# Performance work log

Measured on AMD Instinct MI355X. Metric: run time of the kernel, lower is better.

## Reference

```python
import jax, jax.numpy as jnp
import numpy as np

B, V, T = 64, 196, 64       # batch, visual tokens, text tokens
VIS, TXT, E = 768, 768, 512  # backbone dims, joint embed dim


def l2norm(x):
    return x / jnp.maximum(jnp.linalg.norm(x, axis=-1, keepdims=True), 1e-12)


def setup_inputs() -> dict:
    key = jax.random.key(0)
    ks = jax.random.split(key, 16)
    f = lambda k, s: jax.random.normal(k, s, dtype=jnp.float32)
    return {
        'v_cls': f(ks[0], (B, VIS)),
        'v_tok': f(ks[1], (B, V, VIS)),
        't_cls': f(ks[2], (B, TXT)),
        't_tok': f(ks[3], (B, T, TXT)),
        'Wv_cls': f(ks[4], (VIS, E)) * 0.02, 'bv_cls': jnp.zeros((E,), jnp.float32),
        'Wt_cls': f(ks[5], (TXT, E)) * 0.02, 'bt_cls': jnp.zeros((E,), jnp.float32),
        'Wv_tok': f(ks[6], (VIS, E)) * 0.02, 'bv_tok': jnp.zeros((E,), jnp.float32),
        'Wt_tok': f(ks[7], (TXT, E)) * 0.02, 'bt_tok': jnp.zeros((E,), jnp.float32),
        'wv_fc': f(ks[8], (E,)) * 0.02, 'bv_fc': jnp.zeros((), jnp.float32),
        'wt_fc': f(ks[9], (E,)) * 0.02, 'bt_fc': jnp.zeros((), jnp.float32),
        'text_length': jax.random.randint(ks[10], (B,), 16, T + 1),
    }


def reference(v_cls, v_tok, t_cls, t_tok,
              Wv_cls, bv_cls, Wt_cls, bt_cls,
              Wv_tok, bv_tok, Wt_tok, bt_tok,
              wv_fc, bv_fc, wt_fc, bt_fc, text_length):
    ve_cls = v_cls @ Wv_cls + bv_cls
    te_cls = t_cls @ Wt_cls + bt_cls
    ve = v_tok @ Wv_tok + bv_tok          # [B, V, E]
    te = t_tok @ Wt_tok + bt_tok          # [B, T, E]

    # per-token scalar weights (Linear(E, 1).squeeze(2))
    vw = ve @ wv_fc + bv_fc               # [B, V]
    tw = te @ wt_fc + bt_fc               # [B, T]

    # mask padded text positions (pos >= length), then softmax
    pad = jnp.arange(T)[None, :] >= text_length[:, None]
    tw = jax.nn.softmax(jnp.where(pad, -jnp.inf, tw), axis=-1)
    vw = jax.nn.softmax(vw, axis=-1)

    ve = l2norm(ve)
    te = l2norm(te)

    # full cross-batch token similarity [b, q, v, t]
    sim = jnp.einsum('bvd,qtd->bqvt', ve, te)
    image_to_text = jnp.einsum('bqv,bv->bq', sim.max(axis=-1), vw)
    text_to_image = jnp.einsum('bqt,qt->bq', sim.max(axis=2), tw)

    # diagonal (b == q) similarities drive the cdcr gathers
    sim_diag = jnp.einsum('bvd,btd->bvt', ve, te)
    idx1 = jnp.argmax(sim_diag, axis=-1)   # [B, V] best text token per visual token
    idx2 = jnp.argmax(sim_diag, axis=1)    # [B, T] best visual token per text token
    max_v = jnp.take_along_axis(ve, idx2[:, :, None], axis=1).reshape(-1, E)  # [B*T, E]
    max_t = jnp.take_along_axis(te, idx1[:, :, None], axis=1).reshape(-1, E)  # [B*V, E]

    t_feat = te.reshape(-1, E)
    v_feat = ve.reshape(-1, E)

    def zn(x):  # torch .std() is unbiased (ddof=1)
        return (x - x.mean(axis=0)) / jnp.std(x, axis=0, ddof=1)

    c1 = jnp.einsum('ac,ad,a->cd', zn(t_feat), zn(max_v), tw.reshape(-1)) / B
    c2 = jnp.einsum('ac,ad,a->cd', zn(v_feat), zn(max_t), vw.reshape(-1)) / B
    c = (c1 + c2) / 2.0

    D = c.shape[0]
    on_diag = jnp.sum((jnp.diagonal(c) - 1.0) ** 2)
    off_diag = jnp.sum(c.reshape(-1)[1:].reshape(D - 1, D + 1)[:, :-1] ** 2)
    cdcr_loss = 0.1 * (on_diag * 1.0 + off_diag * 0.06)

    return image_to_text, text_to_image, cdcr_loss
```

## Files before the change

### kernel.cpp

```cpp
#include <hip/hip_runtime.h>
#include <cstddef>

#define EDIM 512
#define KDIM 768
#define NB 64
#define NV 196
#define NT 64
#define MROWS_V (NB * NV)
#define MROWS_T (NB * NT)

typedef __attribute__((ext_vector_type(8))) short bf16x8;
typedef __attribute__((ext_vector_type(4))) float f32x4;

static __device__ inline unsigned short f2bf(float f) {
  unsigned u = __float_as_uint(f);
  unsigned r = (u + 0x7fff + ((u >> 16) & 1)) >> 16;
  return (unsigned short)r;
}
static __device__ inline float bf2f(short s) {
  return __uint_as_float(((unsigned)(unsigned short)s) << 16);
}
static __device__ __forceinline__ int swz4(int r) { return (r + (r >> 2)) & 3; }

static __device__ __forceinline__ void gload16(const void* g, void* l) {
  __builtin_amdgcn_global_load_lds(
      (const __attribute__((address_space(1))) void*)g,
      (__attribute__((address_space(3))) void*)l, 16, 0, 0);
}

__global__ void k_prep(const float* __restrict__ va, short* __restrict__ vo, int na8,
                       const float* __restrict__ ta, short* __restrict__ to, int nb8,
                       const float* __restrict__ W0, const float* __restrict__ W1,
                       short* __restrict__ T0, short* __restrict__ T1) {
  __shared__ float tile[32][33];
  int blk = blockIdx.x;
  int tid = threadIdx.x;
  if (blk < 6240) {
    int i = blk * 256 + tid;
    const float* in; short* outp; int idx;
    if (i < na8) { in = va; outp = vo; idx = i; }
    else { idx = i - na8; if (idx >= nb8) return; in = ta; outp = to; }
    float4 a = *(const float4*)(in + (size_t)idx * 8);
    float4 b = *(const float4*)(in + (size_t)idx * 8 + 4);
    bf16x8 v;
    v[0] = (short)f2bf(a.x); v[1] = (short)f2bf(a.y);
    v[2] = (short)f2bf(a.z); v[3] = (short)f2bf(a.w);
    v[4] = (short)f2bf(b.x); v[5] = (short)f2bf(b.y);
    v[6] = (short)f2bf(b.z); v[7] = (short)f2bf(b.w);
    *(bf16x8*)(outp + (size_t)idx * 8) = v;
  } else {
    int z = blk - 6240;
    int bx = z % 24, by = (z / 24) % 16, bz = z / 384;
    const float* W = bz ? W1 : W0;
    short*       T = bz ? T1 : T0;
    int k0 = bx * 32, n0 = by * 32;
    int tx = tid & 31, ty = tid >> 5;
    for (int i = ty; i < 32; i += 8)
      tile[i][tx] = W[(size_t)(k0 + i) * EDIM + n0 + tx];
    __syncthreads();
    for (int i = ty; i < 32; i += 8)
      T[(size_t)(n0 + i) * KDIM + k0 + tx] = (short)f2bf(tile[tx][i]);
  }
}

__global__ __launch_bounds__(256, 4) void k_proj_mfma2(
    const short* __restrict__ vX, const short* __restrict__ tX,
    const short* __restrict__ WvT, const short* __restrict__ WtT,
    const float* __restrict__ vb, const float* __restrict__ tb,
    short* __restrict__ vout, short* __restrict__ tout) {
  __shared__ short As[2][128 * 32];
  __shared__ short Bs[2][128 * 32];
  int y = blockIdx.y;
  const short* Xbf; const short* WT; const float* bias; short* Mbf; int r0;
  if (y < 98) { Xbf = vX; WT = WvT; bias = vb; Mbf = vout; r0 = y * 128; }
  else        { Xbf = tX; WT = WtT; bias = tb; Mbf = tout; r0 = (y - 98) * 128; }
  int n0 = blockIdx.x * 128;
  int tid = threadIdx.x;
  int w = tid >> 6, lane = tid & 63, lg = lane >> 4, li = lane & 15;
  int fsw = (li + (li >> 2)) & 3;

  const short* aSrc[2];
  const short* bSrc[2];
#pragma unroll
  for (int uu = 0; uu < 2; ++uu) {
    int u = uu * 256 + w * 64 + lane;
    int row = u >> 2, seg = u & 3;
    int ss = seg ^ swz4(row);
    aSrc[uu] = Xbf + (size_t)(r0 + row) * KDIM + ss * 8;
    bSrc[uu] = WT + (size_t)(n0 + row) * KDIM + ss * 8;
  }

  auto stage = [&](int bb) {
    short* Ad = &As[bb][0];
    short* Bd = &Bs[bb][0];
#pragma unroll
    for (int uu = 0; uu < 2; ++uu) {
      gload16(aSrc[uu], Ad + (uu * 256 + w * 64) * 8);
      aSrc[uu] += 32;
      gload16(bSrc[uu], Bd + (uu * 256 + w * 64) * 8);
      bSrc[uu] += 32;
    }
  };

  f32x4 acc[2][8];
#pragma unroll
  for (int i = 0; i < 2; ++i)
#pragma unroll
    for (int j = 0; j < 8; ++j) acc[i][j] = (f32x4){0.f, 0.f, 0.f, 0.f};

  stage(0);
  int cur = 0;
  const int NKC = KDIM / 32;
  for (int kc = 0; kc < NKC; ++kc) {
    __builtin_amdgcn_s_barrier();
    if (kc < NKC - 1) {
      stage(cur ^ 1);
      asm volatile("s_waitcnt vmcnt(4)" ::: "memory");
    } else {
      asm volatile("s_waitcnt vmcnt(0)" ::: "memory");
    }
    __builtin_amdgcn_s_barrier();
    const short* Ab = &As[cur][0];
    const short* Bb = &Bs[cur][0];
    bf16x8 bfr[8];
#pragma unroll
    for (int j = 0; j < 8; ++j)
      bfr[j] = *(const bf16x8*)(Bb + (j * 16 + li) * 32 + (lg ^ fsw) * 8);
    __builtin_amdgcn_s_setprio(1);
#pragma unroll
    for (int i = 0; i < 2; ++i) {
      bf16x8 afr = *(const bf16x8*)(Ab + ((w * 2 + i) * 16 + li) * 32 + (lg ^ fsw) * 8);
#pragma unroll
      for (int j = 0; j < 8; ++j)
        acc[i][j] = __builtin_amdgcn_mfma_f32_16x16x32_bf16(afr, bfr[j], acc[i][j], 0, 0, 0);
    }
    __builtin_amdgcn_s_setprio(0);
    cur ^= 1;
  }
#pragma unroll
  for (int j = 0; j < 8; ++j) {
    int n = n0 + j * 16 + li;
    float bb = bias[n];
#pragma unroll
    for (int i = 0; i < 2; ++i)
#pragma unroll
      for (int reg = 0; reg < 4; ++reg)
        Mbf[(size_t)(r0 + (w * 2 + i) * 16 + lg * 4 + reg) * EDIM + n] =
            (short)f2bf(acc[i][j][reg] + bb);
  }
}

__global__ void k_normfc2(short* __restrict__ vM, short* __restrict__ tM,
                          const float* __restrict__ vfcw, const float* __restrict__ tfcw,
                          const float* __restrict__ vfcb, const float* __restrict__ tfcb,
                          float* __restrict__ vwout, float* __restrict__ twout) {
  int blk = blockIdx.x;
  short* Mbf; const float* fcw; const float* fcb; float* wout; int row;
  if (blk < 3136) { Mbf = vM; fcw = vfcw; fcb = vfcb; wout = vwout;
                    row = blk * 4 + (threadIdx.x >> 6); if (row >= 12544) return; }
  else            { Mbf = tM; fcw = tfcw; fcb = tfcb; wout = twout;
                    row = (blk - 3136) * 4 + (threadIdx.x >> 6); if (row >= 4096) return; }
  int lane = threadIdx.x & 63;
  short* p = Mbf + (size_t)row * EDIM + lane * 8;
  bf16x8 v = *(bf16x8*)p;
  float4 w0 = *(const float4*)(fcw + lane * 8);
  float4 w1 = *(const float4*)(fcw + lane * 8 + 4);
  float a[8];
#pragma unroll
  for (int j = 0; j < 8; ++j) a[j] = bf2f(v[j]);
  float dot = a[0] * w0.x + a[1] * w0.y + a[2] * w0.z + a[3] * w0.w +
              a[4] * w1.x + a[5] * w1.y + a[6] * w1.z + a[7] * w1.w;
  float ss = a[0] * a[0] + a[1] * a[1] + a[2] * a[2] + a[3] * a[3] +
             a[4] * a[4] + a[5] * a[5] + a[6] * a[6] + a[7] * a[7];
  for (int s = 1; s < 64; s <<= 1) {
    dot += __shfl_xor(dot, s);
    ss += __shfl_xor(ss, s);
  }
  float inv = 1.0f / fmaxf(sqrtf(ss), 1e-12f);
#pragma unroll
  for (int j = 0; j < 8; ++j) v[j] = (short)f2bf(a[j] * inv);
  *(bf16x8*)p = v;
  if (lane == 0) wout[row] = dot + fcb[0];
}

__global__ void k_softmax(float* __restrict__ vwf, float* __restrict__ twf,
                          const int* __restrict__ tlen) {
  __shared__ float red[8];
  int tid = threadIdx.x;
  if (blockIdx.x < 64) {
    int b = blockIdx.x;
    float x = (tid < NV) ? vwf[b * NV + tid] : -1e30f;
    float m = x;
    for (int s = 1; s < 64; s <<= 1) m = fmaxf(m, __shfl_xor(m, s));
    if ((tid & 63) == 0) red[tid >> 6] = m;
    __syncthreads();
    m = fmaxf(fmaxf(red[0], red[1]), fmaxf(red[2], red[3]));
    float e = (tid < NV) ? expf(x - m) : 0.0f;
    float s = e;
    for (int st = 1; st < 64; st <<= 1) s += __shfl_xor(s, st);
    if ((tid & 63) == 0) red[4 + (tid >> 6)] = s;
    __syncthreads();
    s = red[4] + red[5] + red[6] + red[7];
    if (tid < NV) vwf[b * NV + tid] = e / s;
  } else {
    int b = blockIdx.x - 64;
    if (tid < 64) {
      int len = tlen[b];
      float x = twf[b * NT + tid];
      bool valid = tid < len;
      float xv = valid ? x : -1e30f;
      float m = xv;
      for (int s = 1; s < 64; s <<= 1) m = fmaxf(m, __shfl_xor(m, s));
      float e = valid ? expf(x - m) : 0.0f;
      float s = e;
      for (int st = 1; st < 64; st <<= 1) s += __shfl_xor(s, st);
      twf[b * NT + tid] = e / s;
    }
  }
}

__global__ __launch_bounds__(512, 4) void k_sim(
    const short* __restrict__ ve_bf, const short* __restrict__ te_bf,
    const float* __restrict__ vwf, const float* __restrict__ twf,
    float* __restrict__ out, int* __restrict__ gMT, int* __restrict__ gMV) {
  __shared__ short As[2][208 * 32];
  __shared__ short Bs[2][128 * 32];
  __shared__ float colv[8][64];
  __shared__ int   coli[8][64];
  __shared__ float redp[8];
  int n = blockIdx.x;
  int xcd = n & 7, idx = n >> 3;
  int b = xcd * 8 + (idx & 7);
  int qq = idx >> 3;
  int tid = threadIdx.x;
  int w = tid >> 6, lane = tid & 63, lg = lane >> 4, li = lane & 15;
  int qsel = w >> 2, wr = w & 3;
  int q = 2 * qq + qsel;
  const short* Abf = ve_bf + (size_t)b * NV * EDIM;
  const short* Bbf = te_bf + (size_t)qq * 128 * EDIM;
  int fsw = (li + (li >> 2)) & 3;
  int nt = wr ? 3 : 4;
  int tbase = wr ? (1 + wr * 3) : 0;

  const short* aSrc[2];
#pragma unroll
  for (int uu = 0; uu < 2; ++uu) {
    int u = uu * 512 + w * 64 + lane;
    int row = u >> 2;
    if (row > NV - 1) row = NV - 1;
    int seg = u & 3;
    int ss = seg ^ swz4(row);
    aSrc[uu] = Abf + (size_t)row * EDIM + ss * 8;
  }
  const short* bSrc;
  {
    int u = tid;
    int row = u >> 2, seg = u & 3;
    int ss = seg ^ swz4(row);
    bSrc = Bbf + (size_t)row * EDIM + ss * 8;
  }

  auto stage = [&](int bb) {
    short* Ad = &As[bb][0];
    short* Bd = &Bs[bb][0];
    gload16(bSrc, Bd + (w * 64) * 8);
    bSrc += 32;
#pragma unroll
    for (int uu = 0; uu < 2; ++uu) {
      int u0 = uu * 512 + w * 64;
      if (u0 < NV * 4) {
        gload16(aSrc[uu], Ad + u0 * 8);
        aSrc[uu] += 32;
      }
    }
  };

  f32x4 acc[4][4];
#pragma unroll
  for (int i = 0; i < 4; ++i)
#pragma unroll
    for (int j = 0; j < 4; ++j) acc[i][j] = (f32x4){0.f, 0.f, 0.f, 0.f};

  stage(0);
  int cur = 0;
  for (int kc = 0; kc < 16; ++kc) {
    __builtin_amdgcn_s_barrier();
    if (kc < 15) {
      stage(cur ^ 1);
      if (w <= 4) asm volatile("s_waitcnt vmcnt(3)" ::: "memory");
      else        asm volatile("s_waitcnt vmcnt(2)" ::: "memory");
    } else {
      asm volatile("s_waitcnt vmcnt(0)" ::: "memory");
    }
    __builtin_amdgcn_s_barrier();
    const short* Ab2 = &As[cur][0];
    const short* Bb2 = &Bs[cur][0];
    bf16x8 bfr[4];
#pragma unroll
    for (int j = 0; j < 4; ++j)
      bfr[j] = *(const bf16x8*)(Bb2 + (qsel * 64 + j * 16 + li) * 32 + (lg ^ fsw) * 8);
    __builtin_amdgcn_s_setprio(1);
#pragma unroll
    for (int i = 0; i < 4; ++i) {
      if (i < nt) {
        bf16x8 afr = *(const bf16x8*)(Ab2 + ((tbase + i) * 16 + li) * 32 + (lg ^ fsw) * 8);
#pragma unroll
        for (int j = 0; j < 4; ++j)
          acc[i][j] = __builtin_amdgcn_mfma_f32_16x16x32_bf16(afr, bfr[j], acc[i][j], 0, 0, 0);
      }
    }
    __builtin_amdgcn_s_setprio(0);
    cur ^= 1;
  }

  bool diag = (b == q);
  bool diagblk = (b >> 1) == qq;
  float ip = 0.f;

  if (diagblk) {
#pragma unroll
    for (int i = 0; i < 4; ++i) {
      if (i < nt) {
#pragma unroll
        for (int reg = 0; reg < 4; ++reg) {
          int v = (tbase + i) * 16 + lg * 4 + reg;
          float m = acc[i][0][reg];
          int ti = li;
#pragma unroll
          for (int j = 1; j < 4; ++j) {
            float vv = acc[i][j][reg];
            int t = j * 16 + li;
            if (vv > m) { m = vv; ti = t; }
          }
          for (int d = 1; d < 16; d <<= 1) {
            float om = __shfl_xor(m, d);
            int oi = __shfl_xor(ti, d);
            if (om > m || (om == m && oi < ti)) { m = om; ti = oi; }
          }
          if (li == 0 && v < NV) {
            ip += vwf[b * NV + v] * m;
            if (diag) gMT[b * NV + v] = b * NT + ti;
          }
        }
      }
    }
    float cm[4]; int cv[4];
#pragma unroll
    for (int j = 0; j < 4; ++j) { cm[j] = -3.0e38f; cv[j] = 0; }
#pragma unroll
    for (int i = 0; i < 4; ++i) {
      if (i < nt) {
#pragma unroll
        for (int reg = 0; reg < 4; ++reg) {
          int v = (tbase + i) * 16 + lg * 4 + reg;
          bool ok = v < NV;
#pragma unroll
          for (int j = 0; j < 4; ++j) {
            float s = ok ? acc[i][j][reg] : -3.0e38f;
            if (s > cm[j]) { cm[j] = s; cv[j] = v; }
          }
        }
      }
    }
#pragma unroll
    for (int j = 0; j < 4; ++j) {
      for (int d = 16; d < 64; d <<= 1) {
        float om = __shfl_xor(cm[j], d);
        int ov = __shfl_xor(cv[j], d);
        if (om > cm[j] || (om == cm[j] && ov < cv[j])) { cm[j] = om; cv[j] = ov; }
      }
      if (lg == 0) { colv[w][j * 16 + li] = cm[j]; coli[w][j * 16 + li] = cv[j]; }
    }
  } else {
#pragma unroll
    for (int i = 0; i < 4; ++i) {
      if (i < nt) {
#pragma unroll
        for (int reg = 0; reg < 4; ++reg) {
          int v = (tbase + i) * 16 + lg * 4 + reg;
          float m = fmaxf(fmaxf(acc[i][0][reg], acc[i][1][reg]),
                          fmaxf(acc[i][2][reg], acc[i][3][reg]));
          for (int d = 1; d < 16; d <<= 1) m = fmaxf(m, __shfl_xor(m, d));
          if (li == 0 && v < NV) ip += vwf[b * NV + v] * m;
        }
      }
    }
    float cm[4];
#pragma unroll
    for (int j = 0; j < 4; ++j) cm[j] = -3.0e38f;
#pragma unroll
    for (int i = 0; i < 4; ++i) {
      if (i < nt) {
#pragma unroll
      for (int reg = 0; reg < 4; ++reg) {
          int v = (tbase + i) * 16 + lg * 4 + reg;
          bool ok = v < NV;
#pragma unroll
          for (int j = 0; j < 4; ++j)
            cm[j] = fmaxf(cm[j], ok ? acc[i][j][reg] : -3.0e38f);
        }
      }
    }
#pragma unroll
    for (int j = 0; j < 4; ++j) {
      for (int d = 16; d < 64; d <<= 1) cm[j] = fmaxf(cm[j], __shfl_xor(cm[j], d));
      if (lg == 0) colv[w][j * 16 + li] = cm[j];
    }
  }
  for (int d = 1; d < 64; d <<= 1) ip += __shfl_xor(ip, d);
  if (lane == 0) redp[w] = ip;
  __syncthreads();
  if (tid < 128) {
    int qs = tid >> 6, t = tid & 63;
    int qe = 2 * qq + qs;
    float m = colv[qs * 4][t];
    if (diagblk) {
      int bi = coli[qs * 4][t];
#pragma unroll
      for (int w2 = 1; w2 < 4; ++w2) {
        float om = colv[qs * 4 + w2][t];
        int ov = coli[qs * 4 + w2][t];
        if (om > m || (om == m && ov < bi)) { m = om; bi = ov; }
      }
      if (b == qe) gMV[b * NT + t] = b * NV + bi;
    } else {
#pragma unroll
      for (int w2 = 1; w2 < 4; ++w2) m = fmaxf(m, colv[qs * 4 + w2][t]);
    }
    float p = twf[qe * NT + t] * m;
    for (int d = 1; d < 64; d <<= 1) p += __shfl_xor(p, d);
    if ((tid & 63) == 0) out[4096 + b * 64 + qe] = p;
  }
  if (tid == 0) {
    out[b * 64 + 2 * qq]     = redp[0] + redp[1] + redp[2] + redp[3];
    out[b * 64 + 2 * qq + 1] = redp[4] + redp[5] + redp[6] + redp[7];
  }
}

__global__ void k_materialize(const short* __restrict__ ve_bf, const short* __restrict__ te_bf,
                              const int* __restrict__ gMT, const int* __restrict__ gMV,
                              const float* __restrict__ vwf, const float* __restrict__ twf,
                              short* __restrict__ tTw, short* __restrict__ mvT,
                              short* __restrict__ vTw, short* __restrict__ mtT,
                              float* __restrict__ statPart) {
  int z = blockIdx.z;
  int at = blockIdx.x, ct = blockIdx.y;
  int K = (z == 2 || z == 3) ? MROWS_V : MROWS_T;
  if (at * 64 >= K) return;
  const short* src; const int* g = 0; short* dst;
  bool applyW;
  const float* wS = (z <= 1) ? twf : vwf;
  if (z == 0)      { src = te_bf; dst = tTw; applyW = true;  }
  else if (z == 1) { src = ve_bf; g = gMV; dst = mvT; applyW = false; }
  else if (z == 2) { src = ve_bf; dst = vTw; applyW = true;  }
  else             { src = te_bf; g = gMT; dst = mtT; applyW = false; }
  __shared__ float tile[64][67];
  __shared__ float wrow[64];
  int tid = threadIdx.x;
  for (int u = tid; u < 512; u += 256) {
    int a = u >> 3, cseg = (u & 7) << 3;
    int ga = at * 64 + a;
    int row = g ? g[ga] : ga;
    bf16x8 vv = *(const bf16x8*)(src + (size_t)row * EDIM + ct * 64 + cseg);
#pragma unroll
    for (int j = 0; j < 8; j++) tile[a][cseg + j] = bf2f(vv[j]);
    if ((u & 7) == 0) wrow[a] = wS[ga];
  }
  __syncthreads();
  for (int u = tid; u < 512; u += 256) {
    int c = u >> 3, aseg = (u & 7) << 3;
    bf16x8 ov;
#pragma unroll
    for (int j = 0; j < 8; j++) {
      float x = tile[aseg + j][c];
      if (applyW) x *= wrow[aseg + j];
      ov[j] = (short)f2bf(x);
    }
    *(bf16x8*)(dst + (size_t)(ct * 64 + c) * K + at * 64 + aseg) = ov;
  }
  int cl = tid >> 2, part = tid & 3;
  float s = 0, ssq = 0, sw = 0;
  for (int a = part * 16; a < part * 16 + 16; ++a) {
    float x = tile[a][cl];
    s += x; ssq += x * x; sw += wrow[a] * x;
  }
  for (int d = 1; d < 4; d <<= 1) {
    s += __shfl_xor(s, d); ssq += __shfl_xor(ssq, d); sw += __shfl_xor(sw, d);
  }
  if (part == 0) {
    int cbase = (z == 0) ? 0 : (z == 1) ? 64 : (z == 2) ? 128 : 324;
    size_t sidx = ((size_t)(cbase + at) * 512 + ct * 64 + cl) * 3;
    statPart[sidx] = s; statPart[sidx + 1] = ssq; statPart[sidx + 2] = sw;
  }
}

__global__ void k_statfin(const float* __restrict__ statPart, float* __restrict__ stats) {
  int m = blockIdx.x, c = threadIdx.x;
  int R = (m < 2) ? MROWS_T : MROWS_V;
  int nchunk = (m < 2) ? 64 : 196;
  int base = (m == 0) ? 0 : (m == 1) ? 64 : (m == 2) ? 128 : 324;
  float s = 0, ss = 0, sw = 0;
  for (int ch = 0; ch < nchunk; ch++) {
    size_t idx = ((size_t)(base + ch) * 512 + c) * 3;
    s += statPart[idx]; ss += statPart[idx + 1]; sw += statPart[idx + 2];
  }
  float mean = s / R;
  float var = (ss - s * mean) / (R - 1);
  float rstd = 1.0f / sqrtf(var);
  stats[(m * 3 + 0) * 512 + c] = mean;
  stats[(m * 3 + 1) * 512 + c] = rstd;
  stats[(m * 3 + 2) * 512 + c] = sw;
}

__global__ __launch_bounds__(256, 4) void k_wgemm2(
    const short* __restrict__ tTw, const short* __restrict__ mvT,
    const short* __restrict__ vTw, const short* __restrict__ mtT,
    float* __restrict__ Spart) {
  __shared__ short As[2][128 * 32];
  __shared__ short Bs[2][128 * 32];
  int c0 = blockIdx.x * 128, d0 = blockIdx.y * 128;
  int z = blockIdx.z;
  int which = z >> 3, slice = z & 7;
  const short* A = which ? vTw : tTw;
  const short* B = which ? mtT : mvT;
  int K = which ? MROWS_V : MROWS_T;
  int nch = (K >> 3) >> 5;
  int a0 = slice * (K >> 3);
  int tid = threadIdx.x;
  int w = tid >> 6, lane = tid & 63, lg = lane >> 4, li = lane & 15;
  int fsw = (li + (li >> 2)) & 3;

  const short* aSrc[2];
  const short* bSrc[2];
#pragma unroll
  for (int uu = 0; uu < 2; ++uu) {
    int u = uu * 256 + w * 64 + lane;
    int row = u >> 2, seg = u & 3;
    int ss = seg ^ swz4(row);
    aSrc[uu] = A + (size_t)(c0 + row) * K + a0 + ss * 8;
    bSrc[uu] = B + (size_t)(d0 + row) * K + a0 + ss * 8;
  }

  auto stage = [&](int bb) {
    short* Ad = &As[bb][0];
    short* Bd = &Bs[bb][0];
#pragma unroll
    for (int uu = 0; uu < 2; ++uu) {
      gload16(aSrc[uu], Ad + (uu * 256 + w * 64) * 8);
      aSrc[uu] += 32;
      gload16(bSrc[uu], Bd + (uu * 256 + w * 64) * 8);
      bSrc[uu] += 32;
    }
  };

  f32x4 acc[2][8];
#pragma unroll
  for (int i = 0; i < 2; ++i)
#pragma unroll
    for (int j = 0; j < 8; ++j) acc[i][j] = (f32x4){0.f, 0.f, 0.f, 0.f};

  stage(0);
  int cur = 0;
  for (int ch = 0; ch < nch; ++ch) {
    __builtin_amdgcn_s_barrier();
    if (ch < nch - 1) {
      stage(cur ^ 1);
      asm volatile("s_waitcnt vmcnt(4)" ::: "memory");
    } else {
      asm volatile("s_waitcnt vmcnt(0)" ::: "memory");
    }
    __builtin_amdgcn_s_barrier();
    const short* Ab = &As[cur][0];
    const short* Bb = &Bs[cur][0];
    bf16x8 bfr[8];
#pragma unroll
    for (int j = 0; j < 8; ++j)
      bfr[j] = *(const bf16x8*)(Bb + (j * 16 + li) * 32 + (lg ^ fsw) * 8);
    __builtin_amdgcn_s_setprio(1);
#pragma unroll
    for (int i = 0; i < 2; ++i) {
      bf16x8 afr = *(const bf16x8*)(Ab + ((w * 2 + i) * 16 + li) * 32 + (lg ^ fsw) * 8);
#pragma unroll
      for (int j = 0; j < 8; ++j)
        acc[i][j] = __builtin_amdgcn_mfma_f32_16x16x32_bf16(afr, bfr[j], acc[i][j], 0, 0, 0);
    }
    __builtin_amdgcn_s_setprio(0);
    cur ^= 1;
  }
  float* outp = Spart + (size_t)z * 512 * 512;
#pragma unroll
  for (int j = 0; j < 8; ++j) {
    int d = d0 + j * 16 + li;
#pragma unroll
    for (int i = 0; i < 2; ++i)
#pragma unroll
      for (int reg = 0; reg < 4; ++reg)
        outp[(size_t)(c0 + (w * 2 + i) * 16 + lg * 4 + reg) * 512 + d] = acc[i][j][reg];
  }
}

__global__ void k_assemble(const float* __restrict__ Spart, const float* __restrict__ stats,
                           float* __restrict__ lossPart) {
  int c = blockIdx.x, tid = threadIdx.x;
  float muT = stats[0 * 512 + c], rsT = stats[1 * 512 + c], swT = stats[2 * 512 + c];
  float muV = stats[6 * 512 + c], rsV = stats[7 * 512 + c], swV = stats[8 * 512 + c];
  const float W = 64.0f, invB = 1.0f / 64.0f;
  float on = 0, off = 0;
  for (int d = tid; d < 512; d += 256) {
    float s1 = 0, s2 = 0;
    for (int sl = 0; sl < 8; sl++) {
      s1 += Spart[((size_t)sl * 512 + c) * 512 + d];
      s2 += Spart[((size_t)(8 + sl) * 512 + c) * 512 + d];
    }
    float muMV = stats[3 * 512 + d], rsMV = stats[4 * 512 + d], swMV = stats[5 * 512 + d];
    float muMT = stats[9 * 512 + d], rsMT = stats[10 * 512 + d], swMT = stats[11 * 512 + d];
    float c1 = (s1 - muT * swMV - muMV * swT + muT * muMV * W) * rsT * rsMV * invB;
    float c2 = (s2 - muV * swMT - muMT * swV + muV * muMT * W) * rsV * rsMT * invB;
    float cc = 0.5f * (c1 + c2);
    if (d == c) { float dd = cc - 1.0f; on += dd * dd; }
    else off += cc * cc;
  }
  __shared__ float r1[4], r2[4];
  for (int s = 1; s < 64; s <<= 1) { on += __shfl_xor(on, s); off += __shfl_xor(off, s); }
  if ((tid & 63) == 0) { r1[tid >> 6] = on; r2[tid >> 6] = off; }
  __syncthreads();
  if (tid == 0) {
    lossPart[c * 2] = r1[0] + r1[1] + r1[2] + r1[3];
    lossPart[c * 2 + 1] = r2[0] + r2[1] + r2[2] + r2[3];
  }
}

__global__ void k_loss(const float* __restrict__ lossPart, float* __restrict__ out) {
  int tid = threadIdx.x;
  float on = 0, off = 0;
  for (int i = tid; i < 512; i += 256) { on += lossPart[2 * i]; off += lossPart[2 * i + 1]; }
  __shared__ float r1[4], r2[4];
  for (int s = 1; s < 64; s <<= 1) { on += __shfl_xor(on, s); off += __shfl_xor(off, s); }
  if ((tid & 63) == 0) { r1[tid >> 6] = on; r2[tid >> 6] = off; }
  __syncthreads();
  if (tid == 0)
    out[8192] = 0.1f * ((r1[0] + r1[1] + r1[2] + r1[3]) +
                        0.06f * (r2[0] + r2[1] + r2[2] + r2[3]));
}

extern "C" void kernel_launch(void* const* d_in, const int* in_sizes, int n_in,
                              void* d_out, int out_size, void* d_ws, size_t ws_size,
                              hipStream_t stream) {
  (void)in_sizes; (void)n_in; (void)out_size; (void)ws_size;
  const float* v_tok  = (const float*)d_in[1];
  const float* t_tok  = (const float*)d_in[3];
  const float* Wv_tok = (const float*)d_in[8];
  const float* Wt_tok = (const float*)d_in[10];
  const float* bv_tok = (const float*)d_in[9];
  const float* bt_tok = (const float*)d_in[11];
  const float* wv_fc  = (const float*)d_in[12];
  const float* bv_fc  = (const float*)d_in[13];
  const float* wt_fc  = (const float*)d_in[14];
  const float* bt_fc  = (const float*)d_in[15];
  const int*   tlen   = (const int*)d_in[16];
  float* out = (float*)d_out;

  char* wsb = (char*)d_ws;
  short* v_tok_bf = (short*)wsb;
  short* t_tok_bf = v_tok_bf + (size_t)9633792;
  short* WvT      = t_tok_bf + (size_t)3145728;
  short* WtT      = WvT + (size_t)393216;
  short* tTw = (short*)wsb;
  short* mvT = tTw + (size_t)2097152;
  short* vTw = mvT + (size_t)2097152;
  short* ve_bf = (short*)(wsb + 27131904);
  short* te_bf = ve_bf + (size_t)6422528;
  float* Spart = (float*)(wsb + 27131904);
  short* mtT = (short*)(wsb + 44171264);
  float* vwf = (float*)(wsb + 57016320);
  float* twf = vwf + 12544;
  int* gMT = (int*)(twf + 4096);
  int* gMV = gMT + 12544;
  float* statPart = (float*)(gMV + 4096);
  float* stats = statPart + (size_t)520 * 512 * 3;
  float* lossPart = stats + 6144;

  k_prep<<<7008, 256, 0, stream>>>(v_tok, v_tok_bf, 1204224, t_tok, t_tok_bf, 393216,
                                   Wv_tok, Wt_tok, WvT, WtT);
  k_proj_mfma2<<<dim3(4, 130), 256, 0, stream>>>(v_tok_bf, t_tok_bf, WvT, WtT,
                                                 bv_tok, bt_tok, ve_bf, te_bf);
  k_normfc2<<<4160, 256, 0, stream>>>(ve_bf, te_bf, wv_fc, wt_fc, bv_fc, bt_fc, vwf, twf);
  k_softmax<<<128, 256, 0, stream>>>(vwf, twf, tlen);
  k_sim<<<2048, 512, 0, stream>>>(ve_bf, te_bf, vwf, twf, out, gMT, gMV);
  k_materialize<<<dim3(196, 8, 4), 256, 0, stream>>>(ve_bf, te_bf, gMT, gMV, vwf, twf,
                                                     tTw, mvT, vTw, mtT, statPart);
  k_statfin<<<4, 512, 0, stream>>>(statPart, stats);
  k_wgemm2<<<dim3(4, 4, 16), 256, 0, stream>>>(tTw, mvT, vTw, mtT, Spart);
  k_assemble<<<512, 256, 0, stream>>>(Spart, stats, lossPart);
  k_loss<<<1, 256, 0, stream>>>(lossPart, out);
}
```

Before: 246.7 us.

## Store transposed operands in K-chunked layout and widen wgemm blocks to 512 threads

New measurement: 247.0 us, median of 2. No clear change (+0.1%).

```diff
diff --git a/kernel.cpp b/kernel.cpp
--- a/kernel.cpp
+++ b/kernel.cpp
@@ -476,7 +476,8 @@
       if (applyW) x *= wrow[aseg + j];
       ov[j] = (short)f2bf(x);
     }
-    *(bf16x8*)(dst + (size_t)(ct * 64 + c) * K + at * 64 + aseg) = ov;
+    int kchunk = at * 2 + (aseg >> 5);
+    *(bf16x8*)(dst + ((size_t)kchunk * 512 + ct * 64 + c) * 32 + (aseg & 31)) = ov;
   }
   int cl = tid >> 2, part = tid & 3;
   float s = 0, ssq = 0, sw = 0;
@@ -512,7 +513,7 @@
   stats[(m * 3 + 2) * 512 + c] = sw;
 }
 
-__global__ __launch_bounds__(256, 4) void k_wgemm2(
+__global__ __launch_bounds__(512, 2) void k_wgemm2(
     const short* __restrict__ tTw, const short* __restrict__ mvT,
     const short* __restrict__ vTw, const short* __restrict__ mtT,
     float* __restrict__ Spart) {
@@ -525,39 +526,29 @@
   const short* B = which ? mtT : mvT;
   int K = which ? MROWS_V : MROWS_T;
   int nch = (K >> 3) >> 5;
-  int a0 = slice * (K >> 3);
+  size_t a0c = (size_t)slice * nch;
   int tid = threadIdx.x;
   int w = tid >> 6, lane = tid & 63, lg = lane >> 4, li = lane & 15;
   int fsw = (li + (li >> 2)) & 3;
 
-  const short* aSrc[2];
-  const short* bSrc[2];
-#pragma unroll
-  for (int uu = 0; uu < 2; ++uu) {
-    int u = uu * 256 + w * 64 + lane;
-    int row = u >> 2, seg = u & 3;
+  const short* aSrc; const short* bSrc;
+  {
+    int row = tid >> 2, seg = tid & 3;
     int ss = seg ^ swz4(row);
-    aSrc[uu] = A + (size_t)(c0 + row) * K + a0 + ss * 8;
-    bSrc[uu] = B + (size_t)(d0 + row) * K + a0 + ss * 8;
+    aSrc = A + (a0c * 512 + (size_t)(c0 + row)) * 32 + ss * 8;
+    bSrc = B + (a0c * 512 + (size_t)(d0 + row)) * 32 + ss * 8;
   }
 
   auto stage = [&](int bb) {
-    short* Ad = &As[bb][0];
-    short* Bd = &Bs[bb][0];
-#pragma unroll
-    for (int uu = 0; uu < 2; ++uu) {
-      gload16(aSrc[uu], Ad + (uu * 256 + w * 64) * 8);
-      aSrc[uu] += 32;
-      gload16(bSrc[uu], Bd + (uu * 256 + w * 64) * 8);
-      bSrc[uu] += 32;
-    }
+    gload16(aSrc, &As[bb][0] + (w * 64) * 8);
+    aSrc += 512 * 32;
+    gload16(bSrc, &Bs[bb][0] + (w * 64) * 8);
+    bSrc += 512 * 32;
   };
 
-  f32x4 acc[2][8];
-#pragma unroll
-  for (int i = 0; i < 2; ++i)
-#pragma unroll
-    for (int j = 0; j < 8; ++j) acc[i][j] = (f32x4){0.f, 0.f, 0.f, 0.f};
+  f32x4 acc[8];
+#pragma unroll
+  for (int j = 0; j < 8; ++j) acc[j] = (f32x4){0.f, 0.f, 0.f, 0.f};
 
   stage(0);
   int cur = 0;
@@ -565,24 +556,19 @@
     __builtin_amdgcn_s_barrier();
     if (ch < nch - 1) {
       stage(cur ^ 1);
-      asm volatile("s_waitcnt vmcnt(4)" ::: "memory");
+      asm volatile("s_waitcnt vmcnt(2)" ::: "memory");
     } else {
       asm volatile("s_waitcnt vmcnt(0)" ::: "memory");
     }
     __builtin_amdgcn_s_barrier();
     const short* Ab = &As[cur][0];
     const short* Bb = &Bs[cur][0];
-    bf16x8 bfr[8];
-#pragma unroll
-    for (int j = 0; j < 8; ++j)
-      bfr[j] = *(const bf16x8*)(Bb + (j * 16 + li) * 32 + (lg ^ fsw) * 8);
+    bf16x8 afr = *(const bf16x8*)(Ab + (w * 16 + li) * 32 + (lg ^ fsw) * 8);
     __builtin_amdgcn_s_setprio(1);
 #pragma unroll
-    for (int i = 0; i < 2; ++i) {
-      bf16x8 afr = *(const bf16x8*)(Ab + ((w * 2 + i) * 16 + li) * 32 + (lg ^ fsw) * 8);
-#pragma unroll
-      for (int j = 0; j < 8; ++j)
-        acc[i][j] = __builtin_amdgcn_mfma_f32_16x16x32_bf16(afr, bfr[j], acc[i][j], 0, 0, 0);
+    for (int j = 0; j < 8; ++j) {
+      bf16x8 bfr = *(const bf16x8*)(Bb + (j * 16 + li) * 32 + (lg ^ fsw) * 8);
+      acc[j] = __builtin_amdgcn_mfma_f32_16x16x32_bf16(afr, bfr, acc[j], 0, 0, 0);
     }
     __builtin_amdgcn_s_setprio(0);
     cur ^= 1;
@@ -592,10 +578,8 @@
   for (int j = 0; j < 8; ++j) {
     int d = d0 + j * 16 + li;
 #pragma unroll
-    for (int i = 0; i < 2; ++i)
-#pragma unroll
-      for (int reg = 0; reg < 4; ++reg)
-        outp[(size_t)(c0 + (w * 2 + i) * 16 + lg * 4 + reg) * 512 + d] = acc[i][j][reg];
+    for (int reg = 0; reg < 4; ++reg)
+      outp[(size_t)(c0 + w * 16 + lg * 4 + reg) * 512 + d] = acc[j][reg];
   }
 }
 
@@ -690,7 +674,7 @@
   k_materialize<<<dim3(196, 8, 4), 256, 0, stream>>>(ve_bf, te_bf, gMT, gMV, vwf, twf,
                                                      tTw, mvT, vTw, mtT, statPart);
   k_statfin<<<4, 512, 0, stream>>>(statPart, stats);
-  k_wgemm2<<<dim3(4, 4, 16), 256, 0, stream>>>(tTw, mvT, vTw, mtT, Spart);
+  k_wgemm2<<<dim3(4, 4, 16), 512, 0, stream>>>(tTw, mvT, vTw, mtT, Spart);
   k_assemble<<<512, 256, 0, stream>>>(Spart, stats, lossPart);
   k_loss<<<1, 256, 0, stream>>>(lossPart, out);
 }
```
